# Kernel tuning notes

Hardware: AMD Instinct MI355X
Metric: run time of the kernel (lower is better)

The kernel has to match this reference:

```python
import jax, jax.numpy as jnp
import numpy as np

N_TOK = 256
C_Z = 128
C = 32
N_HEAD = 4


def setup_inputs() -> dict:
    key = jax.random.key(0)
    ks = jax.random.split(key, 8)
    s = 0.02
    return {
        "z": jax.random.normal(ks[0], (N_TOK, N_TOK, C_Z), dtype=jnp.float32),
        "single_mask": jnp.ones((N_TOK,), dtype=jnp.float32),
        "ln_gamma": jnp.ones((C_Z,), dtype=jnp.float32),
        "ln_beta": jnp.zeros((C_Z,), dtype=jnp.float32),
        "W_q": jax.random.normal(ks[1], (C_Z, N_HEAD * C), dtype=jnp.float32) * s,
        "W_k": jax.random.normal(ks[2], (C_Z, N_HEAD * C), dtype=jnp.float32) * s,
        "W_v": jax.random.normal(ks[3], (C_Z, N_HEAD * C), dtype=jnp.float32) * s,
        "W_b": jax.random.normal(ks[4], (C_Z, N_HEAD), dtype=jnp.float32) * s,
        "W_g": jax.random.normal(ks[5], (C_Z, N_HEAD * C), dtype=jnp.float32) * s,
        "W_out": jax.random.normal(ks[6], (N_HEAD * C, C_Z), dtype=jnp.float32) * s,
    }


def reference(z, single_mask, ln_gamma, ln_beta, W_q, W_k, W_v, W_b, W_g, W_out):
    # LayerNorm over c_z
    mu = jnp.mean(z, axis=-1, keepdims=True)
    var = jnp.var(z, axis=-1, keepdims=True)
    zn = (z - mu) * jax.lax.rsqrt(var + 1e-5) * ln_gamma + ln_beta

    n = zn.shape[0]
    proj = lambda W: (zn @ W).reshape(n, n, N_HEAD, C)
    q = proj(W_q)
    k = proj(W_k)
    v = proj(W_v)
    g = proj(W_g)
    b = zn @ W_b  # [i, j, h] -> used as bias b[j, k, h]

    # a[i,j,k,h] = q[i,j]·k[i,k]/sqrt(c) + b[j,k,h]
    a = jnp.einsum('ijhc,ikhc->ijkh', q, k) / np.sqrt(C).astype(np.float32)
    a = a + b[None, :, :, :]
    a = a + (-1e9) * (1.0 - single_mask)[None, None, :, None]
    a = jax.nn.softmax(a, axis=-2)  # over k

    o = jnp.einsum('ijkh,ikhc->ijhc', a, v)
    o = jax.nn.sigmoid(g) * o
    o = o.reshape(n, n, N_HEAD * C)
    return o @ W_out
```

## Files before the change

kernel.cpp:

```cpp
#include <hip/hip_runtime.h>
#include <hip/hip_bf16.h>

#define NT 256
#define CZ 128
#define CH 32
#define NH 4
#define PL 2097152

typedef unsigned short ushort_t;
typedef unsigned int uint_t;
typedef __attribute__((ext_vector_type(8))) short short8;
typedef __attribute__((ext_vector_type(4))) float f32x4;

__device__ __forceinline__ float bfbits2f(uint_t bits){
  union { uint_t u; float f; } v; v.u = bits; return v.f;
}
__device__ __forceinline__ float bf2f(ushort_t u){
  return bfbits2f(((uint_t)u) << 16);
}
__device__ __forceinline__ ushort_t f2bf(float f){
  union { float f; uint_t u; } v; v.f = f;
  uint_t u = v.u;
  uint_t r = (u + 0x7fffu + ((u >> 16) & 1u)) >> 16;
  return (ushort_t)r;
}
__device__ __forceinline__ void unpk(uint_t w, float& lo, float& hi){
  lo = bfbits2f(w << 16);
  hi = bfbits2f(w & 0xffff0000u);
}
__device__ __forceinline__ short8 as_s8(uint4 u){
  union { uint4 u; short8 s; } v; v.u = u; return v.s;
}
__device__ __forceinline__ int detect_f32(const ushort_t* zz){
  int l = threadIdx.x & 63;
  int bad = 0;
  #pragma unroll
  for(int s=0;s<4;s++){
    float v = bf2f(zz[l*4 + s]);
    if(!(fabsf(v) < 1e9f)) bad = 1;
  }
  return (__ballot(bad) != 0ull) ? 1 : 0;
}

__global__ void k_cvt_small(const void* __restrict__ m_, const void* __restrict__ g_,
    const void* __restrict__ b_, const void* __restrict__ wb_,
    float* __restrict__ dst, const ushort_t* __restrict__ zz){
  int isf32 = detect_f32(zz);
  int idx = threadIdx.x * 4;
  const void* sp; int off;
  if(idx < 256){ sp = m_;  off = idx; }
  else if(idx < 384){ sp = g_;  off = idx-256; }
  else if(idx < 512){ sp = b_;  off = idx-384; }
  else { sp = wb_; off = idx-512; }
  float4 o;
  if(isf32){ o = *(const float4*)((const float*)sp + off); }
  else {
    uint2 u = *(const uint2*)((const ushort_t*)sp + off);
    unpk(u.x, o.x, o.y); unpk(u.y, o.z, o.w);
  }
  *(float4*)(dst + idx) = o;
}

__global__ __launch_bounds__(256) void k_cvt_wt(const void* __restrict__ s0,
    const void* __restrict__ s1, const void* __restrict__ s2,
    const void* __restrict__ s3, const void* __restrict__ s4,
    ushort_t* __restrict__ dst, const ushort_t* __restrict__ zz){
  int isf32 = detect_f32(zz);
  const void* srcs[5] = {s0,s1,s2,s3,s4};
  int w = blockIdx.x >> 6;
  int idx = (blockIdx.x & 63)*256 + threadIdx.x;
  int k = idx >> 7, c = idx & 127;
  const void* sp = srcs[w];
  float v;
  if(isf32) v = ((const float*)sp)[idx];
  else      v = bf2f(((const ushort_t*)sp)[idx]);
  dst[(size_t)w*16384 + (size_t)c*128 + k] = f2bf(v);
}

__global__ __launch_bounds__(256) void k_lnproj(const void* __restrict__ zraw,
    const float* __restrict__ smallf, const ushort_t* __restrict__ Wt,
    ushort_t* __restrict__ qh, ushort_t* __restrict__ kh,
    ushort_t* __restrict__ vh, ushort_t* __restrict__ gh,
    float* __restrict__ btm){
  __shared__ __align__(16) char lds[47104];
  ushort_t* znl = (ushort_t*)lds;
  float*    tbB = (float*)(lds + 34816);
  float*    wbs = (float*)(lds + 45056);
  const float* mkf = smallf;
  const float* gmf = smallf + 256;
  const float* btf = smallf + 384;
  const float* Wbf = smallf + 512;
  int t = threadIdx.x;
  int isf32 = detect_f32((const ushort_t*)zraw);
  wbs[t] = Wbf[t]; wbs[t+256] = Wbf[t+256];
  __syncthreads();

  int row_loc = t >> 1, half = t & 1;
  size_t r = (size_t)blockIdx.x*128 + row_loc;
  float mval = -1e9f * (1.f - mkf[r & 255]);
  float s = 0.f, s2 = 0.f;
  if(isf32){
    const float4* zp = (const float4*)((const float*)zraw + r*CZ + half*64);
    #pragma unroll
    for(int q=0;q<16;q++){
      float4 v = zp[q];
      s  += (v.x + v.y) + (v.z + v.w);
      s2 += (v.x*v.x + v.y*v.y) + (v.z*v.z + v.w*v.w);
    }
  } else {
    const uint4* zp = (const uint4*)((const ushort_t*)zraw + r*CZ + half*64);
    #pragma unroll
    for(int q=0;q<8;q++){
      uint4 u = zp[q];
      const uint_t* pu = (const uint_t*)&u;
      #pragma unroll
      for(int e=0;e<4;e++){
        float lo, hi; unpk(pu[e], lo, hi);
        s += lo + hi; s2 += lo*lo + hi*hi;
      }
    }
  }
  s  += __shfl_xor(s, 1);
  s2 += __shfl_xor(s2, 1);
  float mu  = s * (1.f/CZ);
  float var = fmaxf(s2 * (1.f/CZ) - mu*mu, 0.f);
  float rs  = rsqrtf(var + 1e-5f);
  float acch[4] = {0.f,0.f,0.f,0.f};
  #pragma unroll
  for(int chunk=0;chunk<8;chunk++){
    float v8[8];
    if(isf32){
      const float4* zp = (const float4*)((const float*)zraw + r*CZ + half*64 + chunk*8);
      float4 a = zp[0], b = zp[1];
      v8[0]=a.x; v8[1]=a.y; v8[2]=a.z; v8[3]=a.w;
      v8[4]=b.x; v8[5]=b.y; v8[6]=b.z; v8[7]=b.w;
    } else {
      uint4 u = *(const uint4*)((const ushort_t*)zraw + r*CZ + half*64 + chunk*8);
      const uint_t* pu = (const uint_t*)&u;
      #pragma unroll
      for(int e=0;e<4;e++) unpk(pu[e], v8[e*2], v8[e*2+1]);
    }
    uint_t ow[4];
    #pragma unroll
    for(int e2=0;e2<4;e2++){
      int cg = half*64 + chunk*8 + e2*2;
      float v0 = (v8[e2*2]   - mu)*rs*gmf[cg]   + btf[cg];
      float v1 = (v8[e2*2+1] - mu)*rs*gmf[cg+1] + btf[cg+1];
      float4 w0 = *(const float4*)&wbs[cg*4];
      float4 w1 = *(const float4*)&wbs[(cg+1)*4];
      acch[0] += v0*w0.x + v1*w1.x;
      acch[1] += v0*w0.y + v1*w1.y;
      acch[2] += v0*w0.z + v1*w1.z;
      acch[3] += v0*w0.w + v1*w1.w;
      ow[e2] = (uint_t)f2bf(v0) | ((uint_t)f2bf(v1) << 16);
    }
    uint4 o; o.x=ow[0]; o.y=ow[1]; o.z=ow[2]; o.w=ow[3];
    *(uint4*)(znl + row_loc*136 + half*64 + chunk*8) = o;
  }
  #pragma unroll
  for(int h=0;h<4;h++){
    float tot = acch[h] + __shfl_xor(acch[h], 1);
    if(half == 0) btm[(size_t)h*65536 + r] = tot + mval;
  }
  __syncthreads();

  int wave = t>>6, l = t&63, n = l&15, quad = l>>4;
  uint4 af[2][4];
  #pragma unroll
  for(int mt=0;mt<2;mt++)
    #pragma unroll
    for(int kb=0;kb<4;kb++)
      af[mt][kb] = *(const uint4*)(znl + (wave*32 + mt*16 + n)*136 + kb*32 + quad*8);
  float* T = tbB + wave*640;
  int rrow = l >> 1, rhalf = l & 1;
  ushort_t* outs[4] = {qh, kh, vh, gh};
  size_t row0 = (size_t)blockIdx.x*128 + wave*32;
  #pragma unroll
  for(int w=0;w<4;w++){
    const ushort_t* W = Wt + (size_t)w*16384;
    ushort_t* D = outs[w];
    float sc = (w==0) ? 0.17677669529663687f : 1.f;
    #pragma unroll
    for(int nt=0;nt<8;nt++){
      uint4 bfr[4];
      #pragma unroll
      for(int kb=0;kb<4;kb++)
        bfr[kb] = *(const uint4*)(W + ((size_t)(nt*16 + n))*128 + kb*32 + quad*8);
      f32x4 a0 = {0.f,0.f,0.f,0.f}, a1 = {0.f,0.f,0.f,0.f};
      #pragma unroll
      for(int kb=0;kb<4;kb++){
        a0 = __builtin_amdgcn_mfma_f32_16x16x32_bf16(as_s8(af[0][kb]), as_s8(bfr[kb]), a0, 0,0,0);
        a1 = __builtin_amdgcn_mfma_f32_16x16x32_bf16(as_s8(af[1][kb]), as_s8(bfr[kb]), a1, 0,0,0);
      }
      #pragma unroll
      for(int rr=0;rr<4;rr++){
        T[(quad*4 + rr)*20 + n]      = a0[rr];
        T[(16 + quad*4 + rr)*20 + n] = a1[rr];
      }
      float4 v0 = *(const float4*)(T + rrow*20 + rhalf*8);
      float4 v1 = *(const float4*)(T + rrow*20 + rhalf*8 + 4);
      uint4 o;
      o.x = (uint_t)f2bf(v0.x*sc) | ((uint_t)f2bf(v0.y*sc) << 16);
      o.y = (uint_t)f2bf(v0.z*sc) | ((uint_t)f2bf(v0.w*sc) << 16);
      o.z = (uint_t)f2bf(v1.x*sc) | ((uint_t)f2bf(v1.y*sc) << 16);
      o.w = (uint_t)f2bf(v1.z*sc) | ((uint_t)f2bf(v1.w*sc) << 16);
      *(uint4*)(D + (size_t)(nt>>1)*PL + (row0 + rrow)*CH + (nt&1)*16 + rhalf*8) = o;
    }
  }
}

__global__ __launch_bounds__(256, 4) void k_attn(
    const ushort_t* __restrict__ qh, const ushort_t* __restrict__ kh,
    const ushort_t* __restrict__ vh, const ushort_t* __restrict__ gh,
    const float* __restrict__ btm, ushort_t* __restrict__ oh){
  __shared__ __align__(16) char lds[53248];
  uint4* VfA = (uint4*)lds;
  uint4* Kf  = (uint4*)(lds + 16384);
  ushort_t* Vn = (ushort_t*)(lds + 32768);
  int t = threadIdx.x;
  int i = blockIdx.x >> 2, h = blockIdx.x & 3;
  int wave = t >> 6, l = t & 63;
  int n = l & 15, quad = l >> 4;
  const ushort_t* qhp = qh + (size_t)h*PL + (size_t)(i*NT)*CH;
  const ushort_t* khp = kh + (size_t)h*PL + (size_t)(i*NT)*CH;
  const ushort_t* vhp = vh + (size_t)h*PL + (size_t)(i*NT)*CH;
  const ushort_t* ghp = gh + (size_t)h*PL + (size_t)(i*NT)*CH;
  ushort_t*       ohp = oh + (size_t)h*PL + (size_t)(i*NT)*CH;
  const float*    bth = btm + (size_t)h*65536;

  {
    const uint4* vp = (const uint4*)(vhp + t*CH);
    uint4 u0=vp[0], u1=vp[1], u2=vp[2], u3=vp[3];
    uint4* dstp = (uint4*)(Vn + t*40);
    dstp[0]=u0; dstp[1]=u1; dstp[2]=u2; dstp[3]=u3;
  }
  {
    #pragma unroll
    for(int m=0;m<4;m++){
      int kt = wave*4 + m;
      Kf[kt*64 + l] = *(const uint4*)(khp + (size_t)(kt*16 + n)*CH + quad*8);
    }
  }
  __syncthreads();
  {
    #pragma unroll
    for(int it=0; it<4; it++){
      int u = wave + it*4, kblk = u >> 1, ct = u & 1;
      uint_t d[4];
      #pragma unroll
      for(int e=0;e<4;e++){
        uint_t lo = Vn[(kblk*32 + quad*8 + e*2    )*40 + ct*16 + n];
        uint_t hi = Vn[(kblk*32 + quad*8 + e*2 + 1)*40 + ct*16 + n];
        d[e] = lo | (hi << 16);
      }
      uint4 o; o.x=d[0]; o.y=d[1]; o.z=d[2]; o.w=d[3];
      VfA[u*64 + l] = o;
    }
  }
  __syncthreads();
  ushort_t* Pw = (ushort_t*)(lds + 32768) + wave*2176;

  for(int s=0;s<4;s++){
    int jt = wave*4 + s;
    uint4 qf = *(const uint4*)(qhp + (size_t)(jt*16 + n)*CH + quad*8);
    f32x4 acc[16];
    #pragma unroll
    for(int kt=0;kt<16;kt++)
      acc[kt] = *(const f32x4*)(bth + (size_t)(jt*16 + n)*256 + kt*16 + quad*4);
    #pragma unroll
    for(int kt=0;kt<16;kt++){
      uint4 kfv = Kf[kt*64 + l];
      acc[kt] = __builtin_amdgcn_mfma_f32_16x16x32_bf16(as_s8(kfv), as_s8(qf), acc[kt], 0,0,0);
    }
    float sum0 = 0.f, sum1 = 0.f;
    uint2 pv[16];
    #pragma unroll
    for(int kt=0;kt<16;kt++){
      float e0 = __expf(acc[kt][0]);
      float e1 = __expf(acc[kt][1]);
      float e2 = __expf(acc[kt][2]);
      float e3 = __expf(acc[kt][3]);
      sum0 += e0 + e1; sum1 += e2 + e3;
      pv[kt].x = (uint_t)f2bf(e0) | ((uint_t)f2bf(e1) << 16);
      pv[kt].y = (uint_t)f2bf(e2) | ((uint_t)f2bf(e3) << 16);
    }
    f32x4 oa0 = {0.f,0.f,0.f,0.f}, oa1 = {0.f,0.f,0.f,0.f};
    #pragma unroll
    for(int H=0; H<2; H++){
      #pragma unroll
      for(int kt2=0;kt2<8;kt2++)
        *(uint2*)(Pw + n*136 + kt2*16 + quad*4) = pv[H*8 + kt2];
      #pragma unroll
      for(int kb2=0;kb2<4;kb2++){
        uint4 pf = *(const uint4*)(Pw + n*136 + kb2*32 + quad*8);
        int kg = H*4 + kb2;
        oa0 = __builtin_amdgcn_mfma_f32_16x16x32_bf16(as_s8(VfA[(kg*2+0)*64 + l]), as_s8(pf), oa0, 0,0,0);
        oa1 = __builtin_amdgcn_mfma_f32_16x16x32_bf16(as_s8(VfA[(kg*2+1)*64 + l]), as_s8(pf), oa1, 0,0,0);
      }
    }
    float ssum = sum0 + sum1;
    ssum += __shfl_xor(ssum, 16);
    ssum += __shfl_xor(ssum, 32);
    float inv = 1.f / ssum;
    size_t rb = (size_t)(jt*16 + n)*CH;
    uint2 g0 = *(const uint2*)(ghp + rb + quad*4);
    uint2 g1 = *(const uint2*)(ghp + rb + 16 + quad*4);
    float ga[4], gc[4];
    unpk(g0.x, ga[0], ga[1]); unpk(g0.y, ga[2], ga[3]);
    unpk(g1.x, gc[0], gc[1]); unpk(g1.y, gc[2], gc[3]);
    float v0[4], v1[4];
    #pragma unroll
    for(int rr=0;rr<4;rr++){
      v0[rr] = oa0[rr] * inv * (1.f/(1.f + __expf(-ga[rr])));
      v1[rr] = oa1[rr] * inv * (1.f/(1.f + __expf(-gc[rr])));
    }
    uint2 s0, s1;
    s0.x = (uint_t)f2bf(v0[0]) | ((uint_t)f2bf(v0[1]) << 16);
    s0.y = (uint_t)f2bf(v0[2]) | ((uint_t)f2bf(v0[3]) << 16);
    s1.x = (uint_t)f2bf(v1[0]) | ((uint_t)f2bf(v1[1]) << 16);
    s1.y = (uint_t)f2bf(v1[2]) | ((uint_t)f2bf(v1[3]) << 16);
    *(uint2*)(ohp + rb + quad*4)      = s0;
    *(uint2*)(ohp + rb + 16 + quad*4) = s1;
  }
}

__global__ __launch_bounds__(256) void k_gemm1(const ushort_t* __restrict__ oh,
    const ushort_t* __restrict__ Wt, void* __restrict__ outp,
    const ushort_t* __restrict__ zz){
  __shared__ __align__(16) float tbB[4*640];
  int isf32 = detect_f32(zz);
  int t = threadIdx.x, wave = t>>6, l = t&63, n = l&15, quad = l>>4;
  size_t row0 = (size_t)blockIdx.x*128 + wave*32;
  float* T = tbB + wave*640;
  int rrow = l >> 1, rhalf = l & 1;
  uint4 af[2][4];
  #pragma unroll
  for(int mt=0;mt<2;mt++)
    #pragma unroll
    for(int kb=0;kb<4;kb++)
      af[mt][kb] = *(const uint4*)(oh + (size_t)kb*PL + (row0 + mt*16 + n)*CH + quad*8);
  #pragma unroll
  for(int nt=0;nt<8;nt++){
    uint4 bfr[4];
    #pragma unroll
    for(int kb=0;kb<4;kb++)
      bfr[kb] = *(const uint4*)(Wt + ((size_t)(nt*16 + n))*128 + kb*32 + quad*8);
    f32x4 a0 = {0.f,0.f,0.f,0.f}, a1 = {0.f,0.f,0.f,0.f};
    #pragma unroll
    for(int kb=0;kb<4;kb++){
      a0 = __builtin_amdgcn_mfma_f32_16x16x32_bf16(as_s8(af[0][kb]), as_s8(bfr[kb]), a0, 0,0,0);
      a1 = __builtin_amdgcn_mfma_f32_16x16x32_bf16(as_s8(af[1][kb]), as_s8(bfr[kb]), a1, 0,0,0);
    }
    #pragma unroll
    for(int rr=0;rr<4;rr++){
      T[(quad*4 + rr)*20 + n]      = a0[rr];
      T[(16 + quad*4 + rr)*20 + n] = a1[rr];
    }
    float4 v0 = *(const float4*)(T + rrow*20 + rhalf*8);
    float4 v1 = *(const float4*)(T + rrow*20 + rhalf*8 + 4);
    if(isf32){
      float* of = (float*)outp + (row0 + rrow)*CZ + nt*16 + rhalf*8;
      *(float4*)of = v0;
      *(float4*)(of + 4) = v1;
    } else {
      uint4 o;
      o.x = (uint_t)f2bf(v0.x) | ((uint_t)f2bf(v0.y) << 16);
      o.y = (uint_t)f2bf(v0.z) | ((uint_t)f2bf(v0.w) << 16);
      o.z = (uint_t)f2bf(v1.x) | ((uint_t)f2bf(v1.y) << 16);
      o.w = (uint_t)f2bf(v1.z) | ((uint_t)f2bf(v1.w) << 16);
      *(uint4*)((ushort_t*)outp + (row0 + rrow)*CZ + nt*16 + rhalf*8) = o;
    }
  }
}

extern "C" void kernel_launch(void* const* d_in, const int* in_sizes, int n_in,
                              void* d_out, int out_size, void* d_ws, size_t ws_size,
                              hipStream_t stream){
  char* wsb = (char*)d_ws;
  const size_t TB = (size_t)16777216;
  ushort_t* qh  = (ushort_t*)(wsb);
  ushort_t* kh  = (ushort_t*)(wsb + TB);
  ushort_t* vh  = (ushort_t*)(wsb + 2*TB);
  ushort_t* gh  = (ushort_t*)(wsb + 3*TB);
  ushort_t* oh  = (ushort_t*)(wsb + 4*TB);
  float*    btm = (float*)   (wsb + 5*TB);
  float*  smallf= (float*)   (wsb + 5*TB + (1u<<20));
  ushort_t* Wt  = (ushort_t*)(wsb + 5*TB + (1u<<20) + 4096);
  const ushort_t* zz = (const ushort_t*)d_in[0];

  k_cvt_small<<<1,   256, 0, stream>>>(d_in[1], d_in[2], d_in[3], d_in[7], smallf, zz);
  k_cvt_wt   <<<320, 256, 0, stream>>>(d_in[4], d_in[5], d_in[6], d_in[8], d_in[9], Wt, zz);
  k_lnproj   <<<512, 256, 0, stream>>>(d_in[0], smallf, Wt, qh, kh, vh, gh, btm);
  k_attn     <<<1024,256, 0, stream>>>(qh, kh, vh, gh, btm, oh);
  k_gemm1    <<<512, 256, 0, stream>>>(oh, Wt + (size_t)4*16384, d_out, zz);
}
```

Before: 222.1 us.

## Fold log2e into scores, chunk attention loop, shrink LDS with swizzled P buffer

```diff
diff --git a/kernel.cpp b/kernel.cpp
--- a/kernel.cpp
+++ b/kernel.cpp
@@ -160,7 +160,7 @@
   #pragma unroll
   for(int h=0;h<4;h++){
     float tot = acch[h] + __shfl_xor(acch[h], 1);
-    if(half == 0) btm[(size_t)h*65536 + r] = tot + mval;
+    if(half == 0) btm[(size_t)h*65536 + r] = (tot + mval) * 1.4426950408889634f;
   }
   __syncthreads();
 
@@ -179,7 +179,7 @@
   for(int w=0;w<4;w++){
     const ushort_t* W = Wt + (size_t)w*16384;
     ushort_t* D = outs[w];
-    float sc = (w==0) ? 0.17677669529663687f : 1.f;
+    float sc = (w==0) ? (0.17677669529663687f * 1.4426950408889634f) : 1.f;
     #pragma unroll
     for(int nt=0;nt<8;nt++){
       uint4 bfr[4];
@@ -213,10 +213,11 @@
     const ushort_t* __restrict__ qh, const ushort_t* __restrict__ kh,
     const ushort_t* __restrict__ vh, const ushort_t* __restrict__ gh,
     const float* __restrict__ btm, ushort_t* __restrict__ oh){
-  __shared__ __align__(16) char lds[53248];
-  uint4* VfA = (uint4*)lds;
-  uint4* Kf  = (uint4*)(lds + 16384);
-  ushort_t* Vn = (ushort_t*)(lds + 32768);
+  __shared__ __align__(16) char lds[40960];
+  uint4*    VfA = (uint4*)lds;
+  ushort_t* Pw0 = (ushort_t*)(lds + 16384);
+  uint4*    Kf  = (uint4*)(lds + 24576);
+  ushort_t* Vn  = (ushort_t*)(lds + 16384);
   int t = threadIdx.x;
   int i = blockIdx.x >> 2, h = blockIdx.x & 3;
   int wave = t >> 6, l = t & 63;
@@ -228,19 +229,17 @@
   ushort_t*       ohp = oh + (size_t)h*PL + (size_t)(i*NT)*CH;
   const float*    bth = btm + (size_t)h*65536;
 
+  uint4 kreg[4];
+  #pragma unroll
+  for(int m=0;m<4;m++)
+    kreg[m] = *(const uint4*)(khp + (size_t)((wave*4+m)*16 + n)*CH + quad*8);
+
   {
     const uint4* vp = (const uint4*)(vhp + t*CH);
     uint4 u0=vp[0], u1=vp[1], u2=vp[2], u3=vp[3];
     uint4* dstp = (uint4*)(Vn + t*40);
     dstp[0]=u0; dstp[1]=u1; dstp[2]=u2; dstp[3]=u3;
   }
-  {
-    #pragma unroll
-    for(int m=0;m<4;m++){
-      int kt = wave*4 + m;
-      Kf[kt*64 + l] = *(const uint4*)(khp + (size_t)(kt*16 + n)*CH + quad*8);
-    }
-  }
   __syncthreads();
   {
     #pragma unroll
@@ -258,42 +257,48 @@
     }
   }
   __syncthreads();
-  ushort_t* Pw = (ushort_t*)(lds + 32768) + wave*2176;
+  {
+    #pragma unroll
+    for(int m=0;m<4;m++) Kf[(wave*4+m)*64 + l] = kreg[m];
+  }
+  __syncthreads();
+
+  ushort_t* Pw = Pw0 + wave*1024;
+  int swz = (n & 7) << 4;
 
   for(int s=0;s<4;s++){
     int jt = wave*4 + s;
     uint4 qf = *(const uint4*)(qhp + (size_t)(jt*16 + n)*CH + quad*8);
-    f32x4 acc[16];
-    #pragma unroll
-    for(int kt=0;kt<16;kt++)
-      acc[kt] = *(const f32x4*)(bth + (size_t)(jt*16 + n)*256 + kt*16 + quad*4);
-    #pragma unroll
-    for(int kt=0;kt<16;kt++){
-      uint4 kfv = Kf[kt*64 + l];
-      acc[kt] = __builtin_amdgcn_mfma_f32_16x16x32_bf16(as_s8(kfv), as_s8(qf), acc[kt], 0,0,0);
-    }
+    const float* brow = bth + (size_t)(jt*16 + n)*256 + quad*4;
+    f32x4 oa0 = {0.f,0.f,0.f,0.f}, oa1 = {0.f,0.f,0.f,0.f};
     float sum0 = 0.f, sum1 = 0.f;
-    uint2 pv[16];
-    #pragma unroll
-    for(int kt=0;kt<16;kt++){
-      float e0 = __expf(acc[kt][0]);
-      float e1 = __expf(acc[kt][1]);
-      float e2 = __expf(acc[kt][2]);
-      float e3 = __expf(acc[kt][3]);
-      sum0 += e0 + e1; sum1 += e2 + e3;
-      pv[kt].x = (uint_t)f2bf(e0) | ((uint_t)f2bf(e1) << 16);
-      pv[kt].y = (uint_t)f2bf(e2) | ((uint_t)f2bf(e3) << 16);
-    }
-    f32x4 oa0 = {0.f,0.f,0.f,0.f}, oa1 = {0.f,0.f,0.f,0.f};
-    #pragma unroll
-    for(int H=0; H<2; H++){
-      #pragma unroll
-      for(int kt2=0;kt2<8;kt2++)
-        *(uint2*)(Pw + n*136 + kt2*16 + quad*4) = pv[H*8 + kt2];
-      #pragma unroll
-      for(int kb2=0;kb2<4;kb2++){
-        uint4 pf = *(const uint4*)(Pw + n*136 + kb2*32 + quad*8);
-        int kg = H*4 + kb2;
+    #pragma unroll
+    for(int Q=0;Q<4;Q++){
+      f32x4 acc[4];
+      #pragma unroll
+      for(int m=0;m<4;m++)
+        acc[m] = *(const f32x4*)(brow + (Q*4+m)*16);
+      #pragma unroll
+      for(int m=0;m<4;m++){
+        uint4 kfv = Kf[(Q*4+m)*64 + l];
+        acc[m] = __builtin_amdgcn_mfma_f32_16x16x32_bf16(as_s8(kfv), as_s8(qf), acc[m], 0,0,0);
+      }
+      #pragma unroll
+      for(int m=0;m<4;m++){
+        float e0 = exp2f(acc[m][0]);
+        float e1 = exp2f(acc[m][1]);
+        float e2 = exp2f(acc[m][2]);
+        float e3 = exp2f(acc[m][3]);
+        sum0 += e0 + e1; sum1 += e2 + e3;
+        uint2 pv;
+        pv.x = (uint_t)f2bf(e0) | ((uint_t)f2bf(e1) << 16);
+        pv.y = (uint_t)f2bf(e2) | ((uint_t)f2bf(e3) << 16);
+        *(uint2*)((char*)Pw + (((n<<7) + (m<<5) + (quad<<3)) ^ swz)) = pv;
+      }
+      #pragma unroll
+      for(int kb=0;kb<2;kb++){
+        uint4 pf = *(const uint4*)((char*)Pw + (((n<<7) + (kb<<6) + (quad<<4)) ^ swz));
+        int kg = Q*2 + kb;
         oa0 = __builtin_amdgcn_mfma_f32_16x16x32_bf16(as_s8(VfA[(kg*2+0)*64 + l]), as_s8(pf), oa0, 0,0,0);
         oa1 = __builtin_amdgcn_mfma_f32_16x16x32_bf16(as_s8(VfA[(kg*2+1)*64 + l]), as_s8(pf), oa1, 0,0,0);
       }
```

Measured after the change: 225.4 us. Within noise of the previous version (+1.5%).
